# Performance work log

Measured on AMD Instinct MI355X. Metric: run time of the kernel, lower is better.

## Reference

```python
import jax, jax.numpy as jnp
import numpy as np

N = 100000
E = 640000
C = 128
NEG_SLOPE = 0.2


def _param(key, shape, scale=0.1):
    return jax.random.normal(key, shape, dtype=jnp.float32) * scale


def setup_inputs() -> dict:
    key = jax.random.key(0)
    ks = jax.random.split(key, 20)
    edge_index = jax.random.randint(ks[0], (2, E), 0, N, dtype=jnp.int32)
    emb = jax.random.normal(ks[1], (N, C), dtype=jnp.float32)  # node_embeddings.weight, a=1.0 normal
    d = {"edge_index": edge_index, "emb": emb}
    # per-layer GATv2Conv params: lin_l (W,b), lin_r (W,b), att vector, residual lin (no bias), out bias
    names = ["Wl", "bl", "Wr", "br", "att", "Wres", "bias"]
    shapes = [(C, C), (C,), (C, C), (C,), (C,), (C, C), (C,)]
    i = 2
    for layer in (1, 2):
        for nm, sh in zip(names, shapes):
            d[f"l{layer}_{nm}"] = _param(ks[i], sh)
            i += 1
    return d


def gatv2_layer(x, Wl, bl, Wr, br, att, Wres, bias, src, dst):
    # x: [N,C]; src/dst: [E+N] (self loops included)
    xl = x @ Wl.T + bl                       # source-side transform [N,C]
    xr = x @ Wr.T + br                       # target-side transform [N,C]
    m = jax.nn.leaky_relu(xl[src] + xr[dst], NEG_SLOPE)  # [E',C]
    e = m @ att                               # attention logits [E']
    emax = jax.ops.segment_max(e, dst, num_segments=N)
    ex = jnp.exp(e - emax[dst])
    denom = jax.ops.segment_sum(ex, dst, num_segments=N)
    alpha = ex / denom[dst]                   # segment softmax over incoming edges
    out = jax.ops.segment_sum(alpha[:, None] * xl[src], dst, num_segments=N)
    return out + x @ Wres.T + bias            # residual + bias


def reference(edge_index, emb,
              l1_Wl, l1_bl, l1_Wr, l1_br, l1_att, l1_Wres, l1_bias,
              l2_Wl, l2_bl, l2_Wr, l2_br, l2_att, l2_Wres, l2_bias):
    loops = jnp.arange(N, dtype=edge_index.dtype)
    src = jnp.concatenate([edge_index[0], loops])
    dst = jnp.concatenate([edge_index[1], loops])
    h = gatv2_layer(emb, l1_Wl, l1_bl, l1_Wr, l1_br, l1_att, l1_Wres, l1_bias, src, dst)
    h = jax.nn.relu(h)
    out = gatv2_layer(h, l2_Wl, l2_bl, l2_Wr, l2_br, l2_att, l2_Wres, l2_bias, src, dst)
    return out
```

## Files before the change

### kernel.cpp

```cpp
#include <hip/hip_runtime.h>
#include <math.h>

#define N_NODES 100000
#define N_EDGES 640000
#define C 128
#define CAP 32
#define TILES_PB 3
#define N_TILES ((N_NODES + 63) / 64)

typedef __attribute__((ext_vector_type(8))) short short8;
typedef __attribute__((ext_vector_type(4))) float floatx4;
typedef __attribute__((ext_vector_type(2))) float float2v;
typedef unsigned int uint;
typedef unsigned short ushort;

__device__ __forceinline__ ushort f2bf(float f) {
    union { float f; uint u; } v; v.f = f;
    uint r = v.u + 0x7fffu + ((v.u >> 16) & 1u);
    return (ushort)(r >> 16);
}
__device__ __forceinline__ float2v upk2(uint u) {
    union { uint i; float f; } lo, hi;
    lo.i = u << 16; hi.i = u & 0xffff0000u;
    float2v r; r.x = lo.f; r.y = hi.f; return r;
}
__device__ __forceinline__ float2v fabs2(float2v v) {
    union { float2v f; uint u[2]; } a; a.f = v;
    a.u[0] &= 0x7fffffffu; a.u[1] &= 0x7fffffffu; return a.f;
}
__device__ __forceinline__ float2v fma2(float2v a, float2v b, float2v c) {
    return __builtin_elementwise_fma(a, b, c);
}

__global__ void prep_kernel(const float* __restrict__ w0, const float* __restrict__ w1,
                            const float* __restrict__ w2, const float* __restrict__ w3,
                            const float* __restrict__ w4, const float* __restrict__ w5,
                            ushort* __restrict__ wb, int* __restrict__ cnt) {
    const int bid = blockIdx.x;
    if (bid < 48) {
        int t = bid * 256 + threadIdx.x;
        int m = t >> 11;
        int off = (t & 2047) * 8;
        const float* src = (m == 0) ? w0 : (m == 1) ? w1 : (m == 2) ? w2
                          : (m == 3) ? w3 : (m == 4) ? w4 : w5;
        float4 v0 = *(const float4*)(src + off);
        float4 v1 = *(const float4*)(src + off + 4);
        ushort tmp[8];
        tmp[0] = f2bf(v0.x); tmp[1] = f2bf(v0.y); tmp[2] = f2bf(v0.z); tmp[3] = f2bf(v0.w);
        tmp[4] = f2bf(v1.x); tmp[5] = f2bf(v1.y); tmp[6] = f2bf(v1.z); tmp[7] = f2bf(v1.w);
        *(uint4*)(wb + (size_t)m * 16384 + off) = *(uint4*)tmp;
    } else {
        int idx = (bid - 48) * 256 + threadIdx.x;
        if (idx < N_NODES) cnt[idx] = 0;
    }
}

__global__ void build_kernel(const int* __restrict__ ei, int* __restrict__ cnt,
                             int* __restrict__ colsrc) {
    int i = blockIdx.x * 256 + threadIdx.x;
    if (i >= N_EDGES) return;
    int d = ei[N_EDGES + i];
    int s = ei[i];
    int slot = atomicAdd(&cnt[d], 1);
    if (slot < CAP) colsrc[(size_t)d * CAP + slot] = s;
}

template <int IN_F32, int RES_F32>
__global__ __launch_bounds__(512)
void gemm3_pipe(const void* __restrict__ xin,
                const ushort* __restrict__ wb,
                const float* __restrict__ bl, const float* __restrict__ br,
                const float* __restrict__ bres,
                ushort* __restrict__ xl, ushort* __restrict__ xr,
                void* __restrict__ res) {
    __shared__ ushort xs[2][64][136];
    const int tid = threadIdx.x;
    const int wave = tid >> 6, lane = tid & 63;
    const int quad = lane >> 4, l16 = lane & 15;
    const int col = wave * 16 + l16;
    const int node = tid >> 3;
    const int kc = (tid & 7) * 16;

    short8 bfr[3][4];
    #pragma unroll
    for (int ws = 0; ws < 3; ++ws)
        #pragma unroll
        for (int ks = 0; ks < 4; ++ks)
            bfr[ws][ks] = *(const short8*)(wb + (size_t)ws * 16384 + (size_t)col * 128 + ks * 32 + quad * 8);

    const float bias[3] = { bl[col], br[col], bres[col] };

    const int t0 = blockIdx.x * TILES_PB;

    auto load_tile = [&](int tile, ushort* tmp) {
        const int n = tile * 64 + node;
        if (n < N_NODES) {
            if (IN_F32) {
                const float* src = (const float*)xin + (size_t)n * C + kc;
                float4 v[4];
                #pragma unroll
                for (int i = 0; i < 4; ++i) v[i] = ((const float4*)src)[i];
                #pragma unroll
                for (int i = 0; i < 4; ++i) {
                    tmp[i * 4 + 0] = f2bf(v[i].x); tmp[i * 4 + 1] = f2bf(v[i].y);
                    tmp[i * 4 + 2] = f2bf(v[i].z); tmp[i * 4 + 3] = f2bf(v[i].w);
                }
            } else {
                const ushort* src = (const ushort*)xin + (size_t)n * C + kc;
                *(uint4*)&tmp[0] = *(const uint4*)src;
                *(uint4*)&tmp[8] = *(const uint4*)(src + 8);
            }
        } else {
            #pragma unroll
            for (int i = 0; i < 16; ++i) tmp[i] = 0;
        }
    };

    ushort stg[16];
    load_tile(t0, stg);
    *(uint4*)&xs[0][node][kc]     = *(uint4*)&stg[0];
    *(uint4*)&xs[0][node][kc + 8] = *(uint4*)&stg[8];

    for (int i = 0; i < TILES_PB; ++i) {
        const int tile = t0 + i;
        __syncthreads();

        const bool more = (i + 1 < TILES_PB);
        if (more) load_tile(tile + 1, stg);

        floatx4 acc[4][3];
        #pragma unroll
        for (int rt = 0; rt < 4; ++rt)
            #pragma unroll
            for (int ws = 0; ws < 3; ++ws)
                acc[rt][ws] = (floatx4){0.f, 0.f, 0.f, 0.f};

        #pragma unroll
        for (int rt = 0; rt < 4; ++rt) {
            short8 a[4];
            #pragma unroll
            for (int ks = 0; ks < 4; ++ks)
                a[ks] = *(const short8*)&xs[i & 1][rt * 16 + l16][ks * 32 + quad * 8];
            #pragma unroll
            for (int ws = 0; ws < 3; ++ws)
                #pragma unroll
                for (int ks = 0; ks < 4; ++ks)
                    acc[rt][ws] = __builtin_amdgcn_mfma_f32_16x16x32_bf16(a[ks], bfr[ws][ks], acc[rt][ws], 0, 0, 0);
        }

        if (more) {
            *(uint4*)&xs[(i + 1) & 1][node][kc]     = *(uint4*)&stg[0];
            *(uint4*)&xs[(i + 1) & 1][node][kc + 8] = *(uint4*)&stg[8];
        }

        const int n0 = tile * 64;
        #pragma unroll
        for (int ws = 0; ws < 3; ++ws)
            #pragma unroll
            for (int rt = 0; rt < 4; ++rt)
                #pragma unroll
                for (int r = 0; r < 4; ++r) {
                    int row = n0 + rt * 16 + quad * 4 + r;
                    if (row < N_NODES) {
                        float val = acc[rt][ws][r] + bias[ws];
                        if (ws == 0)      xl[(size_t)row * C + col] = f2bf(val);
                        else if (ws == 1) xr[(size_t)row * C + col] = f2bf(val);
                        else if (RES_F32) ((float*)res)[(size_t)row * C + col] = val;
                        else              ((ushort*)res)[(size_t)row * C + col] = f2bf(val);
                    }
                }
    }
}

template <int OUT_BF16, int RELU, int RES_F32>
__global__ __launch_bounds__(256)
void node_kernel(const ushort* __restrict__ xl, const ushort* __restrict__ xr,
                 const float* __restrict__ att, const int* __restrict__ cnt,
                 const int* __restrict__ colsrc,
                 const void* __restrict__ resin, void* __restrict__ outp) {
    const int tid = threadIdx.x;
    const int gl = tid & 15;
    const int base_c = gl * 8;
    const int d = blockIdx.x * 16 + (tid >> 4);

    float4 at0 = *(const float4*)(att + base_c);
    float4 at1 = *(const float4*)(att + base_c + 4);
    float2v a06[4], a04[4];
    a06[0] = (float2v){0.6f * at0.x, 0.6f * at0.y};
    a06[1] = (float2v){0.6f * at0.z, 0.6f * at0.w};
    a06[2] = (float2v){0.6f * at1.x, 0.6f * at1.y};
    a06[3] = (float2v){0.6f * at1.z, 0.6f * at1.w};
    a04[0] = (float2v){0.4f * at0.x, 0.4f * at0.y};
    a04[1] = (float2v){0.4f * at0.z, 0.4f * at0.w};
    a04[2] = (float2v){0.4f * at1.x, 0.4f * at1.y};
    a04[3] = (float2v){0.4f * at1.z, 0.4f * at1.w};

    uint4 uxr = *(const uint4*)(xr + (size_t)d * C + base_c);
    float2v xr2[4] = { upk2(uxr.x), upk2(uxr.y), upk2(uxr.z), upk2(uxr.w) };

    const int deg0 = cnt[d];
    const int deg = (deg0 < CAP) ? deg0 : CAP;
    const int* cs = colsrc + (size_t)d * CAP;
    const int nch = (deg + 3) >> 2;

    uint4 selfraw = *(const uint4*)(xl + (size_t)d * C + base_c);

    int4 sA = make_int4(d, d, d, d);
    if (deg > 0) sA = *(const int4*)cs;
    sA.x = (0 < deg) ? sA.x : d;
    sA.y = (1 < deg) ? sA.y : d;
    sA.z = (2 < deg) ? sA.z : d;
    sA.w = (3 < deg) ? sA.w : d;
    uint4 R0 = *(const uint4*)(xl + (size_t)sA.x * C + base_c);
    uint4 R1 = *(const uint4*)(xl + (size_t)sA.y * C + base_c);
    uint4 R2 = *(const uint4*)(xl + (size_t)sA.z * C + base_c);
    uint4 R3 = *(const uint4*)(xl + (size_t)sA.w * C + base_c);
    int4 sB = make_int4(d, d, d, d);
    if (deg > 4) sB = *(const int4*)(cs + 4);

    float S;
    float2v O2[4];

    {
        float2v xv[4] = { upk2(selfraw.x), upk2(selfraw.y), upk2(selfraw.z), upk2(selfraw.w) };
        float2v m0 = xv[0] + xr2[0];
        float2v m1 = xv[1] + xr2[1];
        float2v m2 = xv[2] + xr2[2];
        float2v m3 = xv[3] + xr2[3];
        float2v pa = fma2(a06[0], m0, a04[0] * fabs2(m0));
        float2v pb = fma2(a06[1], m1, a04[1] * fabs2(m1));
        pa = fma2(a06[2], m2, fma2(a04[2], fabs2(m2), pa));
        pb = fma2(a06[3], m3, fma2(a04[3], fabs2(m3), pb));
        pa += pb;
        float p = pa.x + pa.y;
        #pragma unroll
        for (int off = 1; off < 16; off <<= 1) p += __shfl_xor(p, off, 64);
        const float w = __expf(p);
        S = w;
        float2v w2 = (float2v){w, w};
        #pragma unroll
        for (int j = 0; j < 4; ++j) O2[j] = w2 * xv[j];
    }

    for (int c = 0; c < nch; ++c) {
        const uint4 c0 = R0, c1 = R1, c2 = R2, c3 = R3;

        const int nb = (c + 1) * 4;
        int4 sN = sB;
        sN.x = (nb + 0 < deg) ? sN.x : d;
        sN.y = (nb + 1 < deg) ? sN.y : d;
        sN.z = (nb + 2 < deg) ? sN.z : d;
        sN.w = (nb + 3 < deg) ? sN.w : d;
        const int bb = (c + 2) * 4;
        if (bb < deg) sB = *(const int4*)(cs + bb);

        R0 = *(const uint4*)(xl + (size_t)sN.x * C + base_c);
        R1 = *(const uint4*)(xl + (size_t)sN.y * C + base_c);
        R2 = *(const uint4*)(xl + (size_t)sN.z * C + base_c);
        R3 = *(const uint4*)(xl + (size_t)sN.w * C + base_c);

        const int e0 = c * 4;
        const uint4 cur[4] = { c0, c1, c2, c3 };
        #pragma unroll
        for (int j = 0; j < 4; ++j) {
            float2v xv[4] = { upk2(cur[j].x), upk2(cur[j].y), upk2(cur[j].z), upk2(cur[j].w) };
            float2v m0 = xv[0] + xr2[0];
            float2v m1 = xv[1] + xr2[1];
            float2v m2 = xv[2] + xr2[2];
            float2v m3 = xv[3] + xr2[3];
            float2v pa = fma2(a06[0], m0, a04[0] * fabs2(m0));
            float2v pb = fma2(a06[1], m1, a04[1] * fabs2(m1));
            pa = fma2(a06[2], m2, fma2(a04[2], fabs2(m2), pa));
            pb = fma2(a06[3], m3, fma2(a04[3], fabs2(m3), pb));
            pa += pb;
            float p = pa.x + pa.y;
            #pragma unroll
            for (int off = 1; off < 16; off <<= 1) p += __shfl_xor(p, off, 64);
            const float w = (e0 + j < deg) ? __expf(p) : 0.f;
            S += w;
            float2v w2 = (float2v){w, w};
            #pragma unroll
            for (int k = 0; k < 4; ++k) O2[k] = fma2(w2, xv[k], O2[k]);
        }
    }

    const float inv = 1.f / S;
    float2v rs[4];
    if (RES_F32) {
        const float* rp = (const float*)resin + (size_t)d * C + base_c;
        float4 q0 = *(const float4*)rp;
        float4 q1 = *(const float4*)(rp + 4);
        rs[0] = (float2v){q0.x, q0.y}; rs[1] = (float2v){q0.z, q0.w};
        rs[2] = (float2v){q1.x, q1.y}; rs[3] = (float2v){q1.z, q1.w};
    } else {
        uint4 urs = *(const uint4*)((const ushort*)resin + (size_t)d * C + base_c);
        rs[0] = upk2(urs.x); rs[1] = upk2(urs.y); rs[2] = upk2(urs.z); rs[3] = upk2(urs.w);
    }
    float2v iv = (float2v){inv, inv};
    float r[8];
    #pragma unroll
    for (int j = 0; j < 4; ++j) {
        float2v rr = fma2(O2[j], iv, rs[j]);
        if (RELU) { rr.x = fmaxf(rr.x, 0.f); rr.y = fmaxf(rr.y, 0.f); }
        r[2 * j] = rr.x; r[2 * j + 1] = rr.y;
    }
    if (OUT_BF16) {
        ushort tmp[8];
        #pragma unroll
        for (int c2 = 0; c2 < 8; ++c2) tmp[c2] = f2bf(r[c2]);
        *((uint4*)((ushort*)outp + (size_t)d * C + base_c)) = *(uint4*)tmp;
    } else {
        float* op = (float*)outp + (size_t)d * C + base_c;
        *(float4*)op       = make_float4(r[0], r[1], r[2], r[3]);
        *(float4*)(op + 4) = make_float4(r[4], r[5], r[6], r[7]);
    }
}

extern "C" void kernel_launch(void* const* d_in, const int* in_sizes, int n_in,
                              void* d_out, int out_size, void* d_ws, size_t ws_size,
                              hipStream_t stream) {
    const int*   ei  = (const int*)d_in[0];
    const float* emb = (const float*)d_in[1];
    const float* L1[7];
    const float* L2[7];
    for (int i = 0; i < 7; ++i) L1[i] = (const float*)d_in[2 + i];
    for (int i = 0; i < 7; ++i) L2[i] = (const float*)d_in[9 + i];
    float* out = (float*)d_out;

    const size_t NC = (size_t)N_NODES * C;
    ushort* xl  = (ushort*)d_ws;
    ushort* xr  = xl + NC;
    ushort* h   = xr + NC;
    ushort* wb  = h + NC;
    int* cnt    = (int*)(wb + 6 * 16384);
    int* colsrc = cnt + N_NODES;

    prep_kernel<<<48 + (N_NODES + 255) / 256, 256, 0, stream>>>(
        L1[0], L1[2], L1[5], L2[0], L2[2], L2[5], wb, cnt);
    build_kernel<<<(N_EDGES + 255) / 256, 256, 0, stream>>>(ei, cnt, colsrc);

    const int gblocks = (N_TILES + TILES_PB - 1) / TILES_PB;
    const int nblocks = N_NODES / 16;

    gemm3_pipe<1, 0><<<gblocks, 512, 0, stream>>>(emb, wb, L1[1], L1[3], L1[6], xl, xr, h);
    node_kernel<1, 1, 0><<<nblocks, 256, 0, stream>>>(xl, xr, L1[4], cnt, colsrc, h, h);

    gemm3_pipe<0, 1><<<gblocks, 512, 0, stream>>>(h, wb + 3 * 16384, L2[1], L2[3], L2[6], xl, xr, out);
    node_kernel<0, 0, 1><<<nblocks, 256, 0, stream>>>(xl, xr, L2[4], cnt, colsrc, out, out);
}
```

Baseline: 316.3 us.

## Fuse all stages into one persistent kernel with grid barriers and degree-sorted nodes

```diff
diff --git a/kernel.cpp b/kernel.cpp
--- a/kernel.cpp
+++ b/kernel.cpp
@@ -5,8 +5,10 @@
 #define N_EDGES 640000
 #define C 128
 #define CAP 32
-#define TILES_PB 3
-#define N_TILES ((N_NODES + 63) / 64)
+#define N_TILES 1563
+#define GRIDB 512
+#define NTHR 512
+#define GT (GRIDB * NTHR)
 
 typedef __attribute__((ext_vector_type(8))) short short8;
 typedef __attribute__((ext_vector_type(4))) float floatx4;
@@ -32,48 +34,29 @@
     return __builtin_elementwise_fma(a, b, c);
 }
 
-__global__ void prep_kernel(const float* __restrict__ w0, const float* __restrict__ w1,
-                            const float* __restrict__ w2, const float* __restrict__ w3,
-                            const float* __restrict__ w4, const float* __restrict__ w5,
-                            ushort* __restrict__ wb, int* __restrict__ cnt) {
-    const int bid = blockIdx.x;
-    if (bid < 48) {
-        int t = bid * 256 + threadIdx.x;
-        int m = t >> 11;
-        int off = (t & 2047) * 8;
-        const float* src = (m == 0) ? w0 : (m == 1) ? w1 : (m == 2) ? w2
-                          : (m == 3) ? w3 : (m == 4) ? w4 : w5;
-        float4 v0 = *(const float4*)(src + off);
-        float4 v1 = *(const float4*)(src + off + 4);
-        ushort tmp[8];
-        tmp[0] = f2bf(v0.x); tmp[1] = f2bf(v0.y); tmp[2] = f2bf(v0.z); tmp[3] = f2bf(v0.w);
-        tmp[4] = f2bf(v1.x); tmp[5] = f2bf(v1.y); tmp[6] = f2bf(v1.z); tmp[7] = f2bf(v1.w);
-        *(uint4*)(wb + (size_t)m * 16384 + off) = *(uint4*)tmp;
-    } else {
-        int idx = (bid - 48) * 256 + threadIdx.x;
-        if (idx < N_NODES) cnt[idx] = 0;
-    }
-}
-
-__global__ void build_kernel(const int* __restrict__ ei, int* __restrict__ cnt,
-                             int* __restrict__ colsrc) {
-    int i = blockIdx.x * 256 + threadIdx.x;
-    if (i >= N_EDGES) return;
-    int d = ei[N_EDGES + i];
-    int s = ei[i];
-    int slot = atomicAdd(&cnt[d], 1);
-    if (slot < CAP) colsrc[(size_t)d * CAP + slot] = s;
+__device__ __forceinline__ void grid_barrier(int* bar) {
+    __syncthreads();
+    if (threadIdx.x == 0) {
+        int* cnt_ = bar;
+        int* gen_ = bar + 1;
+        const int g = __hip_atomic_load(gen_, __ATOMIC_RELAXED, __HIP_MEMORY_SCOPE_AGENT);
+        if (__hip_atomic_fetch_add(cnt_, 1, __ATOMIC_ACQ_REL, __HIP_MEMORY_SCOPE_AGENT) == GRIDB - 1) {
+            __hip_atomic_store(cnt_, 0, __ATOMIC_RELAXED, __HIP_MEMORY_SCOPE_AGENT);
+            __hip_atomic_store(gen_, g + 1, __ATOMIC_RELEASE, __HIP_MEMORY_SCOPE_AGENT);
+        } else {
+            while (__hip_atomic_load(gen_, __ATOMIC_ACQUIRE, __HIP_MEMORY_SCOPE_AGENT) == g)
+                __builtin_amdgcn_s_sleep(2);
+        }
+    }
+    __syncthreads();
 }
 
 template <int IN_F32, int RES_F32>
-__global__ __launch_bounds__(512)
-void gemm3_pipe(const void* __restrict__ xin,
-                const ushort* __restrict__ wb,
-                const float* __restrict__ bl, const float* __restrict__ br,
-                const float* __restrict__ bres,
-                ushort* __restrict__ xl, ushort* __restrict__ xr,
-                void* __restrict__ res) {
-    __shared__ ushort xs[2][64][136];
+__device__ void gemm_stage(const void* __restrict__ xin, const ushort* __restrict__ wb,
+                           const float* __restrict__ bl, const float* __restrict__ br,
+                           const float* __restrict__ bres,
+                           ushort* __restrict__ xl, ushort* __restrict__ xr,
+                           void* __restrict__ res, ushort xs[2][64][136]) {
     const int tid = threadIdx.x;
     const int wave = tid >> 6, lane = tid & 63;
     const int quad = lane >> 4, l16 = lane & 15;
@@ -89,8 +72,6 @@
             bfr[ws][ks] = *(const short8*)(wb + (size_t)ws * 16384 + (size_t)col * 128 + ks * 32 + quad * 8);
 
     const float bias[3] = { bl[col], br[col], bres[col] };
-
-    const int t0 = blockIdx.x * TILES_PB;
 
     auto load_tile = [&](int tile, ushort* tmp) {
         const int n = tile * 64 + node;
@@ -117,16 +98,17 @@
     };
 
     ushort stg[16];
-    load_tile(t0, stg);
+    int t = blockIdx.x;
+    load_tile(t, stg);
     *(uint4*)&xs[0][node][kc]     = *(uint4*)&stg[0];
     *(uint4*)&xs[0][node][kc + 8] = *(uint4*)&stg[8];
 
-    for (int i = 0; i < TILES_PB; ++i) {
-        const int tile = t0 + i;
+    int buf = 0;
+    for (; t < N_TILES; t += GRIDB) {
         __syncthreads();
-
-        const bool more = (i + 1 < TILES_PB);
-        if (more) load_tile(tile + 1, stg);
+        const int tn = t + GRIDB;
+        const bool more = tn < N_TILES;
+        if (more) load_tile(tn, stg);
 
         floatx4 acc[4][3];
         #pragma unroll
@@ -140,7 +122,7 @@
             short8 a[4];
             #pragma unroll
             for (int ks = 0; ks < 4; ++ks)
-                a[ks] = *(const short8*)&xs[i & 1][rt * 16 + l16][ks * 32 + quad * 8];
+                a[ks] = *(const short8*)&xs[buf][rt * 16 + l16][ks * 32 + quad * 8];
             #pragma unroll
             for (int ws = 0; ws < 3; ++ws)
                 #pragma unroll
@@ -149,11 +131,11 @@
         }
 
         if (more) {
-            *(uint4*)&xs[(i + 1) & 1][node][kc]     = *(uint4*)&stg[0];
-            *(uint4*)&xs[(i + 1) & 1][node][kc + 8] = *(uint4*)&stg[8];
-        }
-
-        const int n0 = tile * 64;
+            *(uint4*)&xs[buf ^ 1][node][kc]     = *(uint4*)&stg[0];
+            *(uint4*)&xs[buf ^ 1][node][kc + 8] = *(uint4*)&stg[8];
+        }
+
+        const int n0 = t * 64;
         #pragma unroll
         for (int ws = 0; ws < 3; ++ws)
             #pragma unroll
@@ -169,19 +151,18 @@
                         else              ((ushort*)res)[(size_t)row * C + col] = f2bf(val);
                     }
                 }
+        buf ^= 1;
     }
 }
 
 template <int OUT_BF16, int RELU, int RES_F32>
-__global__ __launch_bounds__(256)
-void node_kernel(const ushort* __restrict__ xl, const ushort* __restrict__ xr,
-                 const float* __restrict__ att, const int* __restrict__ cnt,
-                 const int* __restrict__ colsrc,
-                 const void* __restrict__ resin, void* __restrict__ outp) {
+__device__ void node_stage(const ushort* __restrict__ xl, const ushort* __restrict__ xr,
+                           const float* __restrict__ att, const int* __restrict__ cnt,
+                           const int* __restrict__ colsrc, const int* __restrict__ perm,
+                           const void* __restrict__ resin, void* __restrict__ outp) {
     const int tid = threadIdx.x;
     const int gl = tid & 15;
     const int base_c = gl * 8;
-    const int d = blockIdx.x * 16 + (tid >> 4);
 
     float4 at0 = *(const float4*)(att + base_c);
     float4 at1 = *(const float4*)(att + base_c + 4);
@@ -195,75 +176,37 @@
     a04[2] = (float2v){0.4f * at1.x, 0.4f * at1.y};
     a04[3] = (float2v){0.4f * at1.z, 0.4f * at1.w};
 
-    uint4 uxr = *(const uint4*)(xr + (size_t)d * C + base_c);
-    float2v xr2[4] = { upk2(uxr.x), upk2(uxr.y), upk2(uxr.z), upk2(uxr.w) };
-
-    const int deg0 = cnt[d];
-    const int deg = (deg0 < CAP) ? deg0 : CAP;
-    const int* cs = colsrc + (size_t)d * CAP;
-    const int nch = (deg + 3) >> 2;
-
-    uint4 selfraw = *(const uint4*)(xl + (size_t)d * C + base_c);
-
-    int4 sA = make_int4(d, d, d, d);
-    if (deg > 0) sA = *(const int4*)cs;
-    sA.x = (0 < deg) ? sA.x : d;
-    sA.y = (1 < deg) ? sA.y : d;
-    sA.z = (2 < deg) ? sA.z : d;
-    sA.w = (3 < deg) ? sA.w : d;
-    uint4 R0 = *(const uint4*)(xl + (size_t)sA.x * C + base_c);
-    uint4 R1 = *(const uint4*)(xl + (size_t)sA.y * C + base_c);
-    uint4 R2 = *(const uint4*)(xl + (size_t)sA.z * C + base_c);
-    uint4 R3 = *(const uint4*)(xl + (size_t)sA.w * C + base_c);
-    int4 sB = make_int4(d, d, d, d);
-    if (deg > 4) sB = *(const int4*)(cs + 4);
-
-    float S;
-    float2v O2[4];
-
-    {
-        float2v xv[4] = { upk2(selfraw.x), upk2(selfraw.y), upk2(selfraw.z), upk2(selfraw.w) };
-        float2v m0 = xv[0] + xr2[0];
-        float2v m1 = xv[1] + xr2[1];
-        float2v m2 = xv[2] + xr2[2];
-        float2v m3 = xv[3] + xr2[3];
-        float2v pa = fma2(a06[0], m0, a04[0] * fabs2(m0));
-        float2v pb = fma2(a06[1], m1, a04[1] * fabs2(m1));
-        pa = fma2(a06[2], m2, fma2(a04[2], fabs2(m2), pa));
-        pb = fma2(a06[3], m3, fma2(a04[3], fabs2(m3), pb));
-        pa += pb;
-        float p = pa.x + pa.y;
-        #pragma unroll
-        for (int off = 1; off < 16; off <<= 1) p += __shfl_xor(p, off, 64);
-        const float w = __expf(p);
-        S = w;
-        float2v w2 = (float2v){w, w};
-        #pragma unroll
-        for (int j = 0; j < 4; ++j) O2[j] = w2 * xv[j];
-    }
-
-    for (int c = 0; c < nch; ++c) {
-        const uint4 c0 = R0, c1 = R1, c2 = R2, c3 = R3;
-
-        const int nb = (c + 1) * 4;
-        int4 sN = sB;
-        sN.x = (nb + 0 < deg) ? sN.x : d;
-        sN.y = (nb + 1 < deg) ? sN.y : d;
-        sN.z = (nb + 2 < deg) ? sN.z : d;
-        sN.w = (nb + 3 < deg) ? sN.w : d;
-        const int bb = (c + 2) * 4;
-        if (bb < deg) sB = *(const int4*)(cs + bb);
-
-        R0 = *(const uint4*)(xl + (size_t)sN.x * C + base_c);
-        R1 = *(const uint4*)(xl + (size_t)sN.y * C + base_c);
-        R2 = *(const uint4*)(xl + (size_t)sN.z * C + base_c);
-        R3 = *(const uint4*)(xl + (size_t)sN.w * C + base_c);
-
-        const int e0 = c * 4;
-        const uint4 cur[4] = { c0, c1, c2, c3 };
-        #pragma unroll
-        for (int j = 0; j < 4; ++j) {
-            float2v xv[4] = { upk2(cur[j].x), upk2(cur[j].y), upk2(cur[j].z), upk2(cur[j].w) };
+    for (int i = blockIdx.x * 32 + (tid >> 4); i < N_NODES; i += GRIDB * 32) {
+        const int d = perm[i];
+
+        uint4 uxr = *(const uint4*)(xr + (size_t)d * C + base_c);
+        float2v xr2[4] = { upk2(uxr.x), upk2(uxr.y), upk2(uxr.z), upk2(uxr.w) };
+
+        const int deg0 = cnt[d];
+        const int deg = (deg0 < CAP) ? deg0 : CAP;
+        const int* cs = colsrc + (size_t)d * CAP;
+        const int nch = (deg + 3) >> 2;
+
+        uint4 selfraw = *(const uint4*)(xl + (size_t)d * C + base_c);
+
+        int4 sA = make_int4(d, d, d, d);
+        if (deg > 0) sA = *(const int4*)cs;
+        sA.x = (0 < deg) ? sA.x : d;
+        sA.y = (1 < deg) ? sA.y : d;
+        sA.z = (2 < deg) ? sA.z : d;
+        sA.w = (3 < deg) ? sA.w : d;
+        uint4 R0 = *(const uint4*)(xl + (size_t)sA.x * C + base_c);
+        uint4 R1 = *(const uint4*)(xl + (size_t)sA.y * C + base_c);
+        uint4 R2 = *(const uint4*)(xl + (size_t)sA.z * C + base_c);
+        uint4 R3 = *(const uint4*)(xl + (size_t)sA.w * C + base_c);
+        int4 sB = make_int4(d, d, d, d);
+        if (deg > 4) sB = *(const int4*)(cs + 4);
+
+        float S;
+        float2v O2[4];
+
+        {
+            float2v xv[4] = { upk2(selfraw.x), upk2(selfraw.y), upk2(selfraw.z), upk2(selfraw.w) };
             float2v m0 = xv[0] + xr2[0];
             float2v m1 = xv[1] + xr2[1];
             float2v m2 = xv[2] + xr2[2];
@@ -276,44 +219,159 @@
             float p = pa.x + pa.y;
             #pragma unroll
             for (int off = 1; off < 16; off <<= 1) p += __shfl_xor(p, off, 64);
-            const float w = (e0 + j < deg) ? __expf(p) : 0.f;
-            S += w;
+            const float w = __expf(p);
+            S = w;
             float2v w2 = (float2v){w, w};
             #pragma unroll
-            for (int k = 0; k < 4; ++k) O2[k] = fma2(w2, xv[k], O2[k]);
-        }
-    }
-
-    const float inv = 1.f / S;
-    float2v rs[4];
-    if (RES_F32) {
-        const float* rp = (const float*)resin + (size_t)d * C + base_c;
-        float4 q0 = *(const float4*)rp;
-        float4 q1 = *(const float4*)(rp + 4);
-        rs[0] = (float2v){q0.x, q0.y}; rs[1] = (float2v){q0.z, q0.w};
-        rs[2] = (float2v){q1.x, q1.y}; rs[3] = (float2v){q1.z, q1.w};
-    } else {
-        uint4 urs = *(const uint4*)((const ushort*)resin + (size_t)d * C + base_c);
-        rs[0] = upk2(urs.x); rs[1] = upk2(urs.y); rs[2] = upk2(urs.z); rs[3] = upk2(urs.w);
-    }
-    float2v iv = (float2v){inv, inv};
-    float r[8];
-    #pragma unroll
-    for (int j = 0; j < 4; ++j) {
-        float2v rr = fma2(O2[j], iv, rs[j]);
-        if (RELU) { rr.x = fmaxf(rr.x, 0.f); rr.y = fmaxf(rr.y, 0.f); }
-        r[2 * j] = rr.x; r[2 * j + 1] = rr.y;
-    }
-    if (OUT_BF16) {
+            for (int j = 0; j < 4; ++j) O2[j] = w2 * xv[j];
+        }
+
+        for (int c = 0; c < nch; ++c) {
+            const uint4 cur[4] = { R0, R1, R2, R3 };
+
+            const int nb = (c + 1) * 4;
+            int4 sN = sB;
+            sN.x = (nb + 0 < deg) ? sN.x : d;
+            sN.y = (nb + 1 < deg) ? sN.y : d;
+            sN.z = (nb + 2 < deg) ? sN.z : d;
+            sN.w = (nb + 3 < deg) ? sN.w : d;
+            const int bb = (c + 2) * 4;
+            if (bb < deg) sB = *(const int4*)(cs + bb);
+
+            R0 = *(const uint4*)(xl + (size_t)sN.x * C + base_c);
+            R1 = *(const uint4*)(xl + (size_t)sN.y * C + base_c);
+            R2 = *(const uint4*)(xl + (size_t)sN.z * C + base_c);
+            R3 = *(const uint4*)(xl + (size_t)sN.w * C + base_c);
+
+            const int e0 = c * 4;
+            #pragma unroll
+            for (int j = 0; j < 4; ++j) {
+                float2v xv[4] = { upk2(cur[j].x), upk2(cur[j].y), upk2(cur[j].z), upk2(cur[j].w) };
+                float2v m0 = xv[0] + xr2[0];
+                float2v m1 = xv[1] + xr2[1];
+                float2v m2 = xv[2] + xr2[2];
+                float2v m3 = xv[3] + xr2[3];
+                float2v pa = fma2(a06[0], m0, a04[0] * fabs2(m0));
+                float2v pb = fma2(a06[1], m1, a04[1] * fabs2(m1));
+                pa = fma2(a06[2], m2, fma2(a04[2], fabs2(m2), pa));
+                pb = fma2(a06[3], m3, fma2(a04[3], fabs2(m3), pb));
+                pa += pb;
+                float p = pa.x + pa.y;
+                #pragma unroll
+                for (int off = 1; off < 16; off <<= 1) p += __shfl_xor(p, off, 64);
+                const float w = (e0 + j < deg) ? __expf(p) : 0.f;
+                S += w;
+                float2v w2 = (float2v){w, w};
+                #pragma unroll
+                for (int k = 0; k < 4; ++k) O2[k] = fma2(w2, xv[k], O2[k]);
+            }
+        }
+
+        const float inv = 1.f / S;
+        float2v rs[4];
+        if (RES_F32) {
+            const float* rp = (const float*)resin + (size_t)d * C + base_c;
+            float4 q0 = *(const float4*)rp;
+            float4 q1 = *(const float4*)(rp + 4);
+            rs[0] = (float2v){q0.x, q0.y}; rs[1] = (float2v){q0.z, q0.w};
+            rs[2] = (float2v){q1.x, q1.y}; rs[3] = (float2v){q1.z, q1.w};
+        } else {
+            uint4 urs = *(const uint4*)((const ushort*)resin + (size_t)d * C + base_c);
+            rs[0] = upk2(urs.x); rs[1] = upk2(urs.y); rs[2] = upk2(urs.z); rs[3] = upk2(urs.w);
+        }
+        float2v iv = (float2v){inv, inv};
+        float r[8];
+        #pragma unroll
+        for (int j = 0; j < 4; ++j) {
+            float2v rr = fma2(O2[j], iv, rs[j]);
+            if (RELU) { rr.x = fmaxf(rr.x, 0.f); rr.y = fmaxf(rr.y, 0.f); }
+            r[2 * j] = rr.x; r[2 * j + 1] = rr.y;
+        }
+        if (OUT_BF16) {
+            ushort tmp[8];
+            #pragma unroll
+            for (int c2 = 0; c2 < 8; ++c2) tmp[c2] = f2bf(r[c2]);
+            *((uint4*)((ushort*)outp + (size_t)d * C + base_c)) = *(uint4*)tmp;
+        } else {
+            float* op = (float*)outp + (size_t)d * C + base_c;
+            *(float4*)op       = make_float4(r[0], r[1], r[2], r[3]);
+            *(float4*)(op + 4) = make_float4(r[4], r[5], r[6], r[7]);
+        }
+    }
+}
+
+__global__ __launch_bounds__(NTHR, 4)
+void mega_kernel(const int* __restrict__ ei, const float* __restrict__ emb,
+                 const float* w0, const float* w1, const float* w2,
+                 const float* w3, const float* w4, const float* w5,
+                 const float* b1l, const float* b1r, const float* b1res,
+                 const float* b2l, const float* b2r, const float* b2res,
+                 const float* att1, const float* att2,
+                 ushort* xl, ushort* xr, ushort* h, ushort* wb,
+                 int* cnt, int* gbins, int* gcursor, int* bar,
+                 int* colsrc, int* perm, float* out) {
+    __shared__ __align__(16) ushort xs[2][64][136];
+    __shared__ int lbins[33], lbase[33], gpref[33];
+
+    const int tid = threadIdx.x;
+    const int gtid = blockIdx.x * NTHR + tid;
+
+    if (gtid < 12288) {
+        int m = gtid >> 11;
+        int off = (gtid & 2047) * 8;
+        const float* src = (m == 0) ? w0 : (m == 1) ? w1 : (m == 2) ? w2
+                          : (m == 3) ? w3 : (m == 4) ? w4 : w5;
+        float4 v0 = *(const float4*)(src + off);
+        float4 v1 = *(const float4*)(src + off + 4);
         ushort tmp[8];
-        #pragma unroll
-        for (int c2 = 0; c2 < 8; ++c2) tmp[c2] = f2bf(r[c2]);
-        *((uint4*)((ushort*)outp + (size_t)d * C + base_c)) = *(uint4*)tmp;
-    } else {
-        float* op = (float*)outp + (size_t)d * C + base_c;
-        *(float4*)op       = make_float4(r[0], r[1], r[2], r[3]);
-        *(float4*)(op + 4) = make_float4(r[4], r[5], r[6], r[7]);
-    }
+        tmp[0] = f2bf(v0.x); tmp[1] = f2bf(v0.y); tmp[2] = f2bf(v0.z); tmp[3] = f2bf(v0.w);
+        tmp[4] = f2bf(v1.x); tmp[5] = f2bf(v1.y); tmp[6] = f2bf(v1.z); tmp[7] = f2bf(v1.w);
+        *(uint4*)(wb + (size_t)m * 16384 + off) = *(uint4*)tmp;
+    }
+    for (int i = gtid; i < N_EDGES; i += GT) {
+        int d = ei[N_EDGES + i];
+        int s = ei[i];
+        int slot = atomicAdd(&cnt[d], 1);
+        if (slot < CAP) colsrc[(size_t)d * CAP + slot] = s;
+    }
+    grid_barrier(bar);
+
+    if (tid < 33) lbins[tid] = 0;
+    __syncthreads();
+    int mybin = 0;
+    if (gtid < N_NODES) {
+        int dg = cnt[gtid];
+        mybin = (dg < CAP) ? dg : CAP;
+        atomicAdd(&lbins[mybin], 1);
+    }
+    __syncthreads();
+    if (tid < 33 && lbins[tid]) atomicAdd(&gbins[tid], lbins[tid]);
+    grid_barrier(bar);
+
+    if (tid < 33) lbins[tid] = 0;
+    if (tid == 0) {
+        int s = 0;
+        for (int b = 0; b < 33; ++b) { gpref[b] = s; s += gbins[b]; }
+    }
+    __syncthreads();
+    int myrank = 0;
+    if (gtid < N_NODES) myrank = atomicAdd(&lbins[mybin], 1);
+    __syncthreads();
+    if (tid < 33) lbase[tid] = lbins[tid] ? atomicAdd(&gcursor[tid], lbins[tid]) : 0;
+    __syncthreads();
+    if (gtid < N_NODES) perm[gpref[mybin] + lbase[mybin] + myrank] = gtid;
+    grid_barrier(bar);
+
+    gemm_stage<1, 0>(emb, wb, b1l, b1r, b1res, xl, xr, h, xs);
+    grid_barrier(bar);
+
+    node_stage<1, 1, 0>(xl, xr, att1, cnt, colsrc, perm, h, h);
+    grid_barrier(bar);
+
+    gemm_stage<0, 1>(h, wb + 3 * 16384, b2l, b2r, b2res, xl, xr, out, xs);
+    grid_barrier(bar);
+
+    node_stage<0, 0, 1>(xl, xr, att2, cnt, colsrc, perm, out, out);
 }
 
 extern "C" void kernel_launch(void* const* d_in, const int* in_sizes, int n_in,
@@ -332,19 +390,21 @@
     ushort* xr  = xl + NC;
     ushort* h   = xr + NC;
     ushort* wb  = h + NC;
-    int* cnt    = (int*)(wb + 6 * 16384);
-    int* colsrc = cnt + N_NODES;
-
-    prep_kernel<<<48 + (N_NODES + 255) / 256, 256, 0, stream>>>(
-        L1[0], L1[2], L1[5], L2[0], L2[2], L2[5], wb, cnt);
-    build_kernel<<<(N_EDGES + 255) / 256, 256, 0, stream>>>(ei, cnt, colsrc);
-
-    const int gblocks = (N_TILES + TILES_PB - 1) / TILES_PB;
-    const int nblocks = N_NODES / 16;
-
-    gemm3_pipe<1, 0><<<gblocks, 512, 0, stream>>>(emb, wb, L1[1], L1[3], L1[6], xl, xr, h);
-    node_kernel<1, 1, 0><<<nblocks, 256, 0, stream>>>(xl, xr, L1[4], cnt, colsrc, h, h);
-
-    gemm3_pipe<0, 1><<<gblocks, 512, 0, stream>>>(h, wb + 3 * 16384, L2[1], L2[3], L2[6], xl, xr, out);
-    node_kernel<0, 0, 1><<<nblocks, 256, 0, stream>>>(xl, xr, L2[4], cnt, colsrc, out, out);
-}
+    int* cnt     = (int*)(wb + 6 * 16384);
+    int* gbins   = cnt + N_NODES;
+    int* gcursor = gbins + 33;
+    int* bar     = gcursor + 33;
+    int* colsrc  = bar + 2;
+    int* perm    = colsrc + (size_t)N_NODES * CAP;
+
+    hipMemsetAsync(cnt, 0, (N_NODES + 33 + 33 + 2) * sizeof(int), stream);
+
+    mega_kernel<<<GRIDB, NTHR, 0, stream>>>(
+        ei, emb,
+        L1[0], L1[2], L1[5], L2[0], L2[2], L2[5],
+        L1[1], L1[3], L1[6], L2[1], L2[3], L2[6],
+        L1[4], L2[4],
+        xl, xr, h, wb,
+        cnt, gbins, gcursor, bar,
+        colsrc, perm, out);
+}
```

Result: slower. 940.7 us (+197.4%).
